# Kernel tuning notes

Hardware: AMD Instinct MI355X
Metric: run time of the kernel (lower is better)

The kernel has to match this reference:

```python
import jax, jax.numpy as jnp
import numpy as np


def setup_inputs() -> dict:
    key = jax.random.key(0)
    ks = jax.random.split(key, 7)
    B, Q, K, H, D, R = 2, 2048, 2048, 16, 64, 32
    queries = jax.random.normal(ks[0], (B, Q, H, D), dtype=jnp.float32)
    keys = jax.random.normal(ks[1], (B, K, H, D), dtype=jnp.float32)
    values = jax.random.normal(ks[2], (B, K, H, D), dtype=jnp.float32)
    att_mask = jax.random.randint(ks[3], (B, Q, K), 0, 2, dtype=jnp.int32)
    relative_att_ids = jax.random.randint(ks[4], (B, Q, K), 0, R, dtype=jnp.int32)
    # TruncatedNormal(stddev=0.5) approximated by clipped normal
    relative_emb_table = jnp.clip(
        0.5 * jax.random.normal(ks[5], (R, H, D), dtype=jnp.float32), -1.0, 1.0)
    relative_bias_table = jnp.zeros((R, H), dtype=jnp.float32)
    return {
        'queries': queries,
        'keys': keys,
        'values': values,
        'att_mask': att_mask,
        'relative_att_ids': relative_att_ids,
        'relative_emb_table': relative_emb_table,
        'relative_bias_table': relative_bias_table,
    }


def reference(queries, keys, values, att_mask, relative_att_ids,
              relative_emb_table, relative_bias_table):
    # content scores: [B,Q,K,H]
    content = jnp.einsum('bqhd,bkhd->bqkh', queries, keys)
    # relative scores per vocab id: [B,Q,R,H]
    all_rel = jnp.einsum('bqhd,rhd->bqrh', queries, relative_emb_table)
    all_rel = all_rel + relative_bias_table  # broadcast [R,H]
    # gather along vocab axis per (q,k): [B,Q,K,H]
    rel = jnp.take_along_axis(
        all_rel, relative_att_ids[:, :, :, None].astype(jnp.int32), axis=2)
    scores = content + rel
    d = queries.shape[-1]
    scores = scores / jnp.sqrt(jnp.asarray(d, scores.dtype))
    mask_adder = -10000.0 * (1.0 - att_mask[:, :, :, None].astype(scores.dtype))
    scores = scores + mask_adder
    probs = jax.nn.softmax(scores, axis=-2)  # softmax over key axis
    return jnp.einsum('bqkh,bkhd->bqhd', probs, values)
```

## Files before the change

### kernel.cpp

```cpp
#include <hip/hip_runtime.h>
#include <hip/hip_fp16.h>
#include <stdint.h>

#define Bn 2
#define Qn 2048
#define Kn 2048
#define Hn 16
#define Dn 64
#define Rn 32

#define LOG2E_8 0.18033688011112042f
#define MASK_NEG -14426.950408889634f

typedef __attribute__((ext_vector_type(8))) short short8v;
typedef __attribute__((ext_vector_type(4))) float f32x4;
typedef __attribute__((ext_vector_type(4))) uint32_t u32x4;

static __device__ __forceinline__ uint16_t bf16rn(float f) {
  uint32_t u = __builtin_bit_cast(uint32_t, f);
  u += 0x7FFFu + ((u >> 16) & 1u);
  return (uint16_t)(u >> 16);
}
static __device__ __forceinline__ float bf16f(uint16_t h) {
  uint32_t u = ((uint32_t)h) << 16;
  return __builtin_bit_cast(float, u);
}
static __device__ __forceinline__ float exp2a(float x) {
  float r; asm("v_exp_f32 %0, %1" : "=v"(r) : "v"(x)); return r;
}
static __device__ __forceinline__ uint32_t cvtpk(float lo, float hi) {
  uint32_t r; asm("v_cvt_pk_bf16_f32 %0, %1, %2" : "=v"(r) : "v"(lo), "v"(hi)); return r;
}
static __device__ __forceinline__ void gl_lds16(const void* g, void* l) {
  __builtin_amdgcn_global_load_lds((const __attribute__((address_space(1))) void*)g,
                                   (__attribute__((address_space(3))) void*)l, 16, 0, 0);
}

__global__ void pack_kernel(const int* __restrict__ ids,
                            const int* __restrict__ msk,
                            uint32_t* __restrict__ outp, int n4) {
  int i = blockIdx.x * 256 + threadIdx.x;
  if (i >= n4) return;
  int4 a = reinterpret_cast<const int4*>(ids)[i];
  int4 m = reinterpret_cast<const int4*>(msk)[i];
  uint32_t v = (uint32_t)((a.x | (m.x << 5)) & 0x3f)
             | ((uint32_t)((a.y | (m.y << 5)) & 0x3f) << 8)
             | ((uint32_t)((a.z | (m.z << 5)) & 0x3f) << 16)
             | ((uint32_t)((a.w | (m.w << 5)) & 0x3f) << 24);
  outp[i] = v;
}

__global__ __launch_bounds__(256) void frag_kernel(const float* __restrict__ Kg,
                                                   const float* __restrict__ Vg,
                                                   uint8_t* __restrict__ frag) {
  const int bid = blockIdx.x;
  const int c = bid & 63;
  const int h = (bid >> 6) & 15;
  const int b = bid >> 10;
  uint8_t* panel = frag + (size_t)(b * 16 + h) * 786432u + (size_t)c * 12288u;
  uint4* kf = reinterpret_cast<uint4*>(panel);
  uint4* vf = reinterpret_cast<uint4*>(panel + 8192);
  const int tid = threadIdx.x;
  const int sdq = tid & 7, srow = (tid >> 3) & 15, stile = tid >> 7;
  const int sg = sdq & 3, sdm = sdq >> 2;
  const float* kp = Kg + ((((size_t)b * Kn) + c * 32 + stile * 16 + srow) * Hn + h) * Dn + (sdm * 32 + sg * 4);
  const float4 x0 = *reinterpret_cast<const float4*>(kp);
  const float4 x1 = *reinterpret_cast<const float4*>(kp + 16);
  const float xs0[4] = {x0.x, x0.y, x0.z, x0.w};
  const float xs1[4] = {x1.x, x1.y, x1.z, x1.w};
  uint16_t hh[8], ll[8];
#pragma unroll
  for (int i = 0; i < 4; ++i) {
    const uint16_t h0 = bf16rn(xs0[i]);
    const uint16_t h1 = bf16rn(xs1[i]);
    hh[i] = h0; hh[4 + i] = h1;
    ll[i] = bf16rn(xs0[i] - bf16f(h0));
    ll[4 + i] = bf16rn(xs1[i] - bf16f(h1));
  }
  uint4 uh, ul;
  uh.x = hh[0] | ((uint32_t)hh[1] << 16); uh.y = hh[2] | ((uint32_t)hh[3] << 16);
  uh.z = hh[4] | ((uint32_t)hh[5] << 16); uh.w = hh[6] | ((uint32_t)hh[7] << 16);
  ul.x = ll[0] | ((uint32_t)ll[1] << 16); ul.y = ll[2] | ((uint32_t)ll[3] << 16);
  ul.z = ll[4] | ((uint32_t)ll[5] << 16); ul.w = ll[6] | ((uint32_t)ll[7] << 16);
  kf[(stile * 2 + sdm) * 64 + (srow + 16 * sg)] = uh;
  kf[(4 + stile * 2 + sdm) * 64 + (srow + 16 * sg)] = ul;
  const int vd = tid & 63, vkq = tid >> 6;
  const float* vp = Vg + ((((size_t)b * Kn) + c * 32 + vkq * 4) * Hn + h) * Dn + vd;
  float v0[4], v1[4];
#pragma unroll
  for (int i = 0; i < 4; ++i) {
    v0[i] = vp[i * (Hn * Dn)];
    v1[i] = vp[(16 + i) * (Hn * Dn)];
  }
  uint4 uv;
  uv.x = bf16rn(v0[0]) | ((uint32_t)bf16rn(v0[1]) << 16);
  uv.y = bf16rn(v0[2]) | ((uint32_t)bf16rn(v0[3]) << 16);
  uv.z = bf16rn(v1[0]) | ((uint32_t)bf16rn(v1[1]) << 16);
  uv.w = bf16rn(v1[2]) | ((uint32_t)bf16rn(v1[3]) << 16);
  vf[(vd >> 4) * 64 + (vd & 15) + 16 * vkq] = uv;
}

__global__ __launch_bounds__(256, 2) void attn3_kernel(
    const float* __restrict__ Qg, const float* __restrict__ Eg,
    const float* __restrict__ biasg, const uint8_t* __restrict__ packed,
    const uint8_t* __restrict__ frag, float* __restrict__ outg) {
  __shared__ alignas(16) char smem[66048];
  __half* const tab   = reinterpret_cast<__half*>(smem);
  float* const q_lds  = reinterpret_cast<float*>(smem + 16896);
  float* const et_lds = reinterpret_cast<float*>(smem + 34304);
  char* const cb0 = smem + 16896;
  char* const cb1 = smem + 41472;

  const int tid = threadIdx.x;
  const int lane = tid & 63;
  const int w = tid >> 6;
  const int qr = lane & 15;
  const int g = lane >> 4;

  const int wi = (blockIdx.x & 7) * 64 + (blockIdx.x >> 3);
  const int qt = wi & 15;
  const int h = (wi >> 4) & 15;
  const int b = wi >> 8;
  const int q0 = qt * 128;

  short8v qhi[2][2], qlo[2][2];

#pragma unroll
  for (int half = 0; half < 2; ++half) {
    {
      const int row = tid >> 2, dq = (tid & 3) * 16;
      const float4* s4 = reinterpret_cast<const float4*>(
          Qg + (((size_t)b * Qn + q0 + half * 64 + row) * Hn + h) * Dn + dq);
      float4* dst = reinterpret_cast<float4*>(&q_lds[row * 68 + dq]);
#pragma unroll
      for (int i = 0; i < 4; ++i) dst[i] = s4[i];
    }
    if (half == 0) {
      const int r = tid >> 3, d0 = (tid & 7) * 8;
      const float* src = Eg + ((r * Hn + h) * Dn + d0);
#pragma unroll
      for (int i = 0; i < 8; ++i) et_lds[(d0 + i) * 33 + r] = src[i];
    }
    __syncthreads();
#pragma unroll
    for (int t = 0; t < 2; ++t) {
      const int ql = w * 32 + t * 16 + qr;
      if ((ql >> 6) == half) {
        const int rl = ql & 63;
#pragma unroll
        for (int dm = 0; dm < 2; ++dm) {
#pragma unroll
          for (int j = 0; j < 8; ++j) {
            const int dl = (j < 4) ? (4 * g + j) : (16 + 4 * g + (j - 4));
            const float x = q_lds[rl * 68 + dm * 32 + dl];
            const uint16_t hi = bf16rn(x);
            qhi[t][dm][j] = (short)hi;
            qlo[t][dm][j] = (short)bf16rn(x - bf16f(hi));
          }
        }
      }
    }
    {
      const int r = tid & 31, q8 = tid >> 5;
      float a8[8] = {0.f, 0.f, 0.f, 0.f, 0.f, 0.f, 0.f, 0.f};
      const float bias = biasg[r * Hn + h];
      for (int d = 0; d < 64; ++d) {
        const float e = et_lds[d * 33 + r];
#pragma unroll
        for (int i = 0; i < 8; ++i) a8[i] += e * q_lds[(q8 * 8 + i) * 68 + d];
      }
#pragma unroll
      for (int i = 0; i < 8; ++i) {
        const float ar = LOG2E_8 * (a8[i] + bias);
        const int qq = half * 64 + q8 * 8 + i;
        tab[qq * 66 + r]      = __float2half(ar + MASK_NEG);
        tab[qq * 66 + 32 + r] = __float2half(ar);
      }
    }
    __syncthreads();
  }

  const uint8_t* panel = frag + (size_t)(b * 16 + h) * 786432u;
  const uint8_t* sbase = panel + (size_t)w * 3072 + (size_t)lane * 16;

  const int64_t prow0 = ((int64_t)(b * Qn + q0 + w * 32 + qr)) * Kn + 4 * g;
  const int64_t prow1 = prow0 + (int64_t)16 * Kn;
  const int trow0 = (w * 32 + qr) * 66;
  const int trow1 = trow0 + 16 * 66;

  uint32_t pc[2][4], pn[2][4];
#pragma unroll
  for (int j = 0; j < 4; ++j) {
    pc[0][j] = *(const uint32_t*)(packed + prow0 + j * 16);
    pc[1][j] = *(const uint32_t*)(packed + prow1 + j * 16);
  }

  char* cbc = cb0;
  char* cbn = cb1;
#pragma unroll
  for (int sub = 0; sub < 2; ++sub) {
    const uint8_t* gs = sbase + sub * 12288;
    char* ld = cbc + sub * 12288 + w * 3072;
    gl_lds16(gs, ld); gl_lds16(gs + 1024, ld + 1024); gl_lds16(gs + 2048, ld + 2048);
  }
  asm volatile("s_waitcnt vmcnt(0)" ::: "memory");
  __syncthreads();

  f32x4 acc[2][4] = {{{0.f,0.f,0.f,0.f},{0.f,0.f,0.f,0.f},{0.f,0.f,0.f,0.f},{0.f,0.f,0.f,0.f}},
                     {{0.f,0.f,0.f,0.f},{0.f,0.f,0.f,0.f},{0.f,0.f,0.f,0.f},{0.f,0.f,0.f,0.f}}};
  float mrun[2] = {-1e30f, -1e30f};
  float lrun[2] = {0.f, 0.f};

  for (int c = 0; c < 32; ++c) {
    if (c + 1 < 32) {
#pragma unroll
      for (int sub = 0; sub < 2; ++sub) {
        const uint8_t* gs = sbase + (size_t)(2 * (c + 1) + sub) * 12288u;
        char* ld = cbn + sub * 12288 + w * 3072;
        gl_lds16(gs, ld); gl_lds16(gs + 1024, ld + 1024); gl_lds16(gs + 2048, ld + 2048);
      }
      const int64_t kb = (int64_t)(c + 1) * 64;
#pragma unroll
      for (int j = 0; j < 4; ++j) {
        pn[0][j] = *(const uint32_t*)(packed + prow0 + kb + j * 16);
        pn[1][j] = *(const uint32_t*)(packed + prow1 + kb + j * 16);
      }
    }

    const short8v* kbase = reinterpret_cast<const short8v*>(cbc);
    f32x4 s[2][4] = {{{0.f,0.f,0.f,0.f},{0.f,0.f,0.f,0.f},{0.f,0.f,0.f,0.f},{0.f,0.f,0.f,0.f}},
                     {{0.f,0.f,0.f,0.f},{0.f,0.f,0.f,0.f},{0.f,0.f,0.f,0.f},{0.f,0.f,0.f,0.f}}};
    __builtin_amdgcn_s_setprio(1);
#pragma unroll
    for (int sub = 0; sub < 2; ++sub) {
      const int sb = sub * 768;
#pragma unroll
      for (int dm = 0; dm < 2; ++dm) {
        const short8v k0h = kbase[sb + dm * 64 + lane];
        const short8v k1h = kbase[sb + (2 + dm) * 64 + lane];
        const short8v k0l = kbase[sb + (4 + dm) * 64 + lane];
        const short8v k1l = kbase[sb + (6 + dm) * 64 + lane];
        const int j0 = sub * 2, j1 = sub * 2 + 1;
        s[0][j0] = __builtin_amdgcn_mfma_f32_16x16x32_bf16(k0h, qhi[0][dm], s[0][j0], 0, 0, 0);
        s[0][j0] = __builtin_amdgcn_mfma_f32_16x16x32_bf16(k0l, qhi[0][dm], s[0][j0], 0, 0, 0);
        s[0][j0] = __builtin_amdgcn_mfma_f32_16x16x32_bf16(k0h, qlo[0][dm], s[0][j0], 0, 0, 0);
        s[0][j1] = __builtin_amdgcn_mfma_f32_16x16x32_bf16(k1h, qhi[0][dm], s[0][j1], 0, 0, 0);
        s[0][j1] = __builtin_amdgcn_mfma_f32_16x16x32_bf16(k1l, qhi[0][dm], s[0][j1], 0, 0, 0);
        s[0][j1] = __builtin_amdgcn_mfma_f32_16x16x32_bf16(k1h, qlo[0][dm], s[0][j1], 0, 0, 0);
        s[1][j0] = __builtin_amdgcn_mfma_f32_16x16x32_bf16(k0h, qhi[1][dm], s[1][j0], 0, 0, 0);
        s[1][j0] = __builtin_amdgcn_mfma_f32_16x16x32_bf16(k0l, qhi[1][dm], s[1][j0], 0, 0, 0);
        s[1][j0] = __builtin_amdgcn_mfma_f32_16x16x32_bf16(k0h, qlo[1][dm], s[1][j0], 0, 0, 0);
        s[1][j1] = __builtin_amdgcn_mfma_f32_16x16x32_bf16(k1h, qhi[1][dm], s[1][j1], 0, 0, 0);
        s[1][j1] = __builtin_amdgcn_mfma_f32_16x16x32_bf16(k1l, qhi[1][dm], s[1][j1], 0, 0, 0);
        s[1][j1] = __builtin_amdgcn_mfma_f32_16x16x32_bf16(k1h, qlo[1][dm], s[1][j1], 0, 0, 0);
      }
    }
    __builtin_amdgcn_s_setprio(0);

    short8v vv[2][4];
#pragma unroll
    for (int sub = 0; sub < 2; ++sub) {
      const short8v* vb = reinterpret_cast<const short8v*>(cbc + sub * 12288 + 8192);
#pragma unroll
      for (int dt = 0; dt < 4; ++dt) vv[sub][dt] = vb[dt * 64 + lane];
    }

#pragma unroll
    for (int t = 0; t < 2; ++t) {
      const int trow = t ? trow1 : trow0;
      float sv[16];
#pragma unroll
      for (int i = 0; i < 16; ++i) {
        const int j = i >> 2, r = i & 3;
        const uint32_t v = (pc[t][j] >> (8 * r)) & 63u;
        sv[i] = fmaf(LOG2E_8, s[t][j][r], __half2float(tab[trow + (int)v]));
      }
      float mx = fmaxf(fmaxf(fmaxf(sv[0], sv[1]), fmaxf(sv[2], sv[3])),
                       fmaxf(fmaxf(sv[4], sv[5]), fmaxf(sv[6], sv[7])));
      mx = fmaxf(mx, fmaxf(fmaxf(fmaxf(sv[8], sv[9]), fmaxf(sv[10], sv[11])),
                           fmaxf(fmaxf(sv[12], sv[13]), fmaxf(sv[14], sv[15]))));
      mx = fmaxf(mx, __shfl_xor(mx, 16));
      mx = fmaxf(mx, __shfl_xor(mx, 32));
      if (__any(mx > mrun[t] + 8.f)) {
        const float mnew = fmaxf(mrun[t], mx);
        const float sc = exp2a(mrun[t] - mnew);
        mrun[t] = mnew;
        f32x4 scv;
        scv[0] = __shfl(sc, 4 * g + 0); scv[1] = __shfl(sc, 4 * g + 1);
        scv[2] = __shfl(sc, 4 * g + 2); scv[3] = __shfl(sc, 4 * g + 3);
        acc[t][0] *= scv; acc[t][1] *= scv; acc[t][2] *= scv; acc[t][3] *= scv;
        lrun[t] *= sc;
      }
      float pv[16];
      float ps = 0.f;
#pragma unroll
      for (int i = 0; i < 16; ++i) { pv[i] = exp2a(sv[i] - mrun[t]); ps += pv[i]; }
      lrun[t] += ps;
      u32x4 pu0, pu1;
      pu0[0] = cvtpk(pv[0], pv[1]);  pu0[1] = cvtpk(pv[2], pv[3]);
      pu0[2] = cvtpk(pv[4], pv[5]);  pu0[3] = cvtpk(pv[6], pv[7]);
      pu1[0] = cvtpk(pv[8], pv[9]);  pu1[1] = cvtpk(pv[10], pv[11]);
      pu1[2] = cvtpk(pv[12], pv[13]); pu1[3] = cvtpk(pv[14], pv[15]);
      const short8v pa0 = __builtin_bit_cast(short8v, pu0);
      const short8v pa1 = __builtin_bit_cast(short8v, pu1);
      __builtin_amdgcn_s_setprio(1);
#pragma unroll
      for (int dt = 0; dt < 4; ++dt) {
        acc[t][dt] = __builtin_amdgcn_mfma_f32_16x16x32_bf16(pa0, vv[0][dt], acc[t][dt], 0, 0, 0);
        acc[t][dt] = __builtin_amdgcn_mfma_f32_16x16x32_bf16(pa1, vv[1][dt], acc[t][dt], 0, 0, 0);
      }
      __builtin_amdgcn_s_setprio(0);
    }

#pragma unroll
    for (int j = 0; j < 4; ++j) { pc[0][j] = pn[0][j]; pc[1][j] = pn[1][j]; }

    asm volatile("s_waitcnt vmcnt(0)" ::: "memory");
    __syncthreads();
    char* tmp = cbc; cbc = cbn; cbn = tmp;
  }

#pragma unroll
  for (int t = 0; t < 2; ++t) {
    float lt = lrun[t];
    lt += __shfl_xor(lt, 16);
    lt += __shfl_xor(lt, 32);
    const float linv = 1.0f / lt;
    f32x4 lv;
    lv[0] = __shfl(linv, 4 * g + 0); lv[1] = __shfl(linv, 4 * g + 1);
    lv[2] = __shfl(linv, 4 * g + 2); lv[3] = __shfl(linv, 4 * g + 3);
#pragma unroll
    for (int dt = 0; dt < 4; ++dt) {
#pragma unroll
      for (int r = 0; r < 4; ++r) {
        const int qrow = q0 + w * 32 + t * 16 + 4 * g + r;
        outg[(((size_t)b * Qn + qrow) * Hn + h) * Dn + dt * 16 + qr] = acc[t][dt][r] * lv[r];
      }
    }
  }
}

__global__ __launch_bounds__(256) void attn_old_kernel(
    const float* __restrict__ Qg, const float* __restrict__ Kg,
    const float* __restrict__ Vg, const int* __restrict__ maskg,
    const int* __restrict__ idsg, const float* __restrict__ Eg,
    const float* __restrict__ biasg, float* __restrict__ outg) {
  __shared__ alignas(16) char smem[34304];
  float* const allrel = reinterpret_cast<float*>(smem);
  float* const q_lds  = reinterpret_cast<float*>(smem + 8448);
  float* const et_lds = reinterpret_cast<float*>(smem + 25856);
  uint4* const kfrag  = reinterpret_cast<uint4*>(smem + 8448);
  uint4* const vfrag  = reinterpret_cast<uint4*>(smem + 16640);

  const int tid  = threadIdx.x;
  const int lane = tid & 63;
  const int w    = tid >> 6;
  const int qr   = lane & 15;
  const int g    = lane >> 4;

  const int bid = blockIdx.x;
  const int h  = bid & 15;
  const int qt = (bid >> 4) & 31;
  const int b  = bid >> 9;
  const int q0 = qt * 64;

  {
    const int row = tid >> 2, dq = (tid & 3) * 16;
    const float4* s4 =
        reinterpret_cast<const float4*>(Qg + (((b * Qn) + q0 + row) * Hn + h) * Dn + dq);
    float4* dst = reinterpret_cast<float4*>(&q_lds[row * 68 + dq]);
#pragma unroll
    for (int i = 0; i < 4; ++i) dst[i] = s4[i];
  }
  {
    const int r = tid >> 3, d0 = (tid & 7) * 8;
    const float* src = Eg + ((r * Hn + h) * Dn + d0);
#pragma unroll
    for (int i = 0; i < 8; ++i) et_lds[(d0 + i) * 33 + r] = src[i];
  }
  __syncthreads();

  const int qloc = w * 16 + qr;
  short8v qhi[2], qlo[2];
#pragma unroll
  for (int dm = 0; dm < 2; ++dm) {
#pragma unroll
    for (int j = 0; j < 8; ++j) {
      const int dl = (j < 4) ? (4 * g + j) : (16 + 4 * g + (j - 4));
      const float x = q_lds[qloc * 68 + dm * 32 + dl];
      const uint16_t hi = bf16rn(x);
      qhi[dm][j] = (short)hi;
      qlo[dm][j] = (short)bf16rn(x - bf16f(hi));
    }
  }

  {
    const int r = tid & 31, q8 = tid >> 5;
    float acc[8] = {0.f, 0.f, 0.f, 0.f, 0.f, 0.f, 0.f, 0.f};
    const float bias = biasg[r * Hn + h];
    for (int d = 0; d < 64; ++d) {
      const float e = et_lds[d * 33 + r];
#pragma unroll
      for (int i = 0; i < 8; ++i) acc[i] += e * q_lds[(q8 * 8 + i) * 68 + d];
    }
#pragma unroll
    for (int i = 0; i < 8; ++i)
      allrel[(q8 * 8 + i) * 33 + r] = 0.125f * (acc[i] + bias);
  }
  __syncthreads();

  const int sdq = tid & 7, srow = (tid >> 3) & 15, stile = tid >> 7;
  const int sg = sdq & 3, sdm = sdq >> 2;
  int koff = (((b * Kn) + stile * 16 + srow) * Hn + h) * Dn + (sdm * 32 + sg * 4);
  const int kslotH = (stile * 2 + sdm) * 64 + (srow + 16 * sg);
  const int kslotL = (4 + stile * 2 + sdm) * 64 + (srow + 16 * sg);
  const int vd = tid & 63, vkq = tid >> 6;
  int voff = (((b * Kn) + vkq * 4) * Hn + h) * Dn + vd;
  const int vslot = (vd >> 4) * 64 + (vd & 15) + 16 * vkq;

  const int qglob = q0 + qloc;
  const int prow = (b * Qn + qglob) * Kn + 4 * g;

  f32x4 acc[4] = {{0.f,0.f,0.f,0.f},{0.f,0.f,0.f,0.f},{0.f,0.f,0.f,0.f},{0.f,0.f,0.f,0.f}};
  float mrun = -1e30f, lrun = 0.f;

  const short8v* kfs = reinterpret_cast<const short8v*>(kfrag);
  const short8v* vfs = reinterpret_cast<const short8v*>(vfrag);

  for (int c = 0; c < 64; ++c) {
    const int kb = c * 32;
    __syncthreads();
    {
      const float4 x0 = *reinterpret_cast<const float4*>(Kg + koff);
      const float4 x1 = *reinterpret_cast<const float4*>(Kg + koff + 16);
      koff += 32 * Hn * Dn;
      const float xs0[4] = {x0.x, x0.y, x0.z, x0.w};
      const float xs1[4] = {x1.x, x1.y, x1.z, x1.w};
      uint16_t hh[8], ll[8];
#pragma unroll
      for (int i = 0; i < 4; ++i) {
        const uint16_t h0 = bf16rn(xs0[i]);
        const uint16_t h1 = bf16rn(xs1[i]);
        hh[i] = h0; hh[4 + i] = h1;
        ll[i] = bf16rn(xs0[i] - bf16f(h0));
        ll[4 + i] = bf16rn(xs1[i] - bf16f(h1));
      }
      uint4 uh, ul;
      uh.x = hh[0] | ((uint32_t)hh[1] << 16); uh.y = hh[2] | ((uint32_t)hh[3] << 16);
      uh.z = hh[4] | ((uint32_t)hh[5] << 16); uh.w = hh[6] | ((uint32_t)hh[7] << 16);
      ul.x = ll[0] | ((uint32_t)ll[1] << 16); ul.y = ll[2] | ((uint32_t)ll[3] << 16);
      ul.z = ll[4] | ((uint32_t)ll[5] << 16); ul.w = ll[6] | ((uint32_t)ll[7] << 16);
      kfrag[kslotH] = uh;
      kfrag[kslotL] = ul;
    }
    {
      float v0[4], v1[4];
#pragma unroll
      for (int i = 0; i < 4; ++i) {
        v0[i] = Vg[voff + i * (Hn * Dn)];
        v1[i] = Vg[voff + 16 * Hn * Dn + i * (Hn * Dn)];
      }
      voff += 32 * Hn * Dn;
      uint4 uv;
      uv.x = bf16rn(v0[0]) | ((uint32_t)bf16rn(v0[1]) << 16);
      uv.y = bf16rn(v0[2]) | ((uint32_t)bf16rn(v0[3]) << 16);
      uv.z = bf16rn(v1[0]) | ((uint32_t)bf16rn(v1[1]) << 16);
      uv.w = bf16rn(v1[2]) | ((uint32_t)bf16rn(v1[3]) << 16);
      vfrag[vslot] = uv;
    }
    __syncthreads();

    f32x4 s0 = {0.f, 0.f, 0.f, 0.f}, s1 = {0.f, 0.f, 0.f, 0.f};
#pragma unroll
    for (int dm = 0; dm < 2; ++dm) {
      const short8v k0h = kfs[(dm) * 64 + lane];
      const short8v k1h = kfs[(2 + dm) * 64 + lane];
      const short8v k0l = kfs[(4 + dm) * 64 + lane];
      const short8v k1l = kfs[(6 + dm) * 64 + lane];
      s0 = __builtin_amdgcn_mfma_f32_16x16x32_bf16(k0h, qhi[dm], s0, 0, 0, 0);
      s1 = __builtin_amdgcn_mfma_f32_16x16x32_bf16(k1h, qhi[dm], s1, 0, 0, 0);
      s0 = __builtin_amdgcn_mfma_f32_16x16x32_bf16(k0h, qlo[dm], s0, 0, 0, 0);
      s1 = __builtin_amdgcn_mfma_f32_16x16x32_bf16(k1h, qlo[dm], s1, 0, 0, 0);
      s0 = __builtin_amdgcn_mfma_f32_16x16x32_bf16(k0l, qhi[dm], s0, 0, 0, 0);
      s1 = __builtin_amdgcn_mfma_f32_16x16x32_bf16(k1l, qhi[dm], s1, 0, 0, 0);
    }

    float sv[8];
    {
      const int ib = prow + kb;
      const int4 i0 = *reinterpret_cast<const int4*>(idsg + ib);
      const int4 i1 = *reinterpret_cast<const int4*>(idsg + ib + 16);
      const int4 m0 = *reinterpret_cast<const int4*>(maskg + ib);
      const int4 m1 = *reinterpret_cast<const int4*>(maskg + ib + 16);
      const int ia0[4] = {i0.x, i0.y, i0.z, i0.w};
      const int ia1[4] = {i1.x, i1.y, i1.z, i1.w};
      const int ma0[4] = {m0.x, m0.y, m0.z, m0.w};
      const int ma1[4] = {m1.x, m1.y, m1.z, m1.w};
#pragma unroll
      for (int r = 0; r < 4; ++r) {
        sv[r]     = 0.125f * s0[r] + allrel[qloc * 33 + ia0[r]] + (ma0[r] ? 0.f : -10000.f);
        sv[4 + r] = 0.125f * s1[r] + allrel[qloc * 33 + ia1[r]] + (ma1[r] ? 0.f : -10000.f);
      }
    }

    float m8 = sv[0];
#pragma unroll
    for (int i = 1; i < 8; ++i) m8 = fmaxf(m8, sv[i]);
    m8 = fmaxf(m8, __shfl_xor(m8, 16));
    m8 = fmaxf(m8, __shfl_xor(m8, 32));
    const float mnew = fmaxf(mrun, m8);
    const float sc = __expf(mrun - mnew);
    mrun = mnew;
    float pv[8];
    float ps = 0.f;
#pragma unroll
    for (int i = 0; i < 8; ++i) { pv[i] = __expf(sv[i] - mnew); ps += pv[i]; }
    ps += __shfl_xor(ps, 16);
    ps += __shfl_xor(ps, 32);
    lrun = lrun * sc + ps;

    f32x4 scv;
#pragma unroll
    for (int r = 0; r < 4; ++r) scv[r] = __shfl(sc, 4 * g + r);
#pragma unroll
    for (int dt = 0; dt < 4; ++dt) acc[dt] *= scv;

    short8v pa;
#pragma unroll
    for (int i = 0; i < 8; ++i) pa[i] = (short)bf16rn(pv[i]);
#pragma unroll
    for (int dt = 0; dt < 4; ++dt)
      acc[dt] = __builtin_amdgcn_mfma_f32_16x16x32_bf16(pa, vfs[dt * 64 + lane], acc[dt], 0, 0, 0);
  }

  const float linv = 1.0f / lrun;
  f32x4 lv;
#pragma unroll
  for (int r = 0; r < 4; ++r) lv[r] = __shfl(linv, 4 * g + r);
#pragma unroll
  for (int dt = 0; dt < 4; ++dt) {
#pragma unroll
    for (int r = 0; r < 4; ++r) {
      const int qrow = q0 + w * 16 + 4 * g + r;
      outg[(((b * Qn) + qrow) * Hn + h) * Dn + dt * 16 + qr] = acc[dt][r] * lv[r];
    }
  }
}

extern "C" void kernel_launch(void* const* d_in, const int* in_sizes, int n_in,
                              void* d_out, int out_size, void* d_ws, size_t ws_size,
                              hipStream_t stream) {
  const float* Qg    = (const float*)d_in[0];
  const float* Kg    = (const float*)d_in[1];
  const float* Vg    = (const float*)d_in[2];
  const int*   maskg = (const int*)d_in[3];
  const int*   idsg  = (const int*)d_in[4];
  const float* Eg    = (const float*)d_in[5];
  const float* biasg = (const float*)d_in[6];
  float* outg = (float*)d_out;

  const size_t needPack = (size_t)Bn * Qn * Kn;
  const size_t needFrag = (size_t)Bn * Hn * 64 * 12288;
  const int n4 = (Bn * Qn * Kn) / 4;

  if (ws_size >= needPack + needFrag) {
    pack_kernel<<<n4 / 256, 256, 0, stream>>>(idsg, maskg, (uint32_t*)d_ws, n4);
    frag_kernel<<<Bn * Hn * 64, 256, 0, stream>>>(Kg, Vg, (uint8_t*)d_ws + needPack);
    attn3_kernel<<<Bn * Hn * (Qn / 128), 256, 0, stream>>>(
        Qg, Eg, biasg, (const uint8_t*)d_ws, (const uint8_t*)d_ws + needPack, outg);
  } else {
    attn_old_kernel<<<Bn * Hn * (Qn / 64), 256, 0, stream>>>(
        Qg, Kg, Vg, maskg, idsg, Eg, biasg, outg);
  }
}
```

Baseline: 130.0 us.

## Drop split-bf16 QK and online max, accumulate row sums via MFMA

QK^T now uses single bf16 operands instead of the hi/lo split, so each tile needs a third of the MFMAs and half the K fragment bytes. The log2e/8 scale is folded into K during fragment packing. The running-max rescaling is removed and exp2 is applied directly, which assumes scores stay bounded. Row sums come from an extra MFMA against a ones vector instead of scalar adds and shuffles. This trades accuracy and overflow safety for fewer matrix ops, less memory traffic and less VALU work, and it also prefetches the first K/V tile before the Q setup.

```diff
diff --git a/kernel.cpp b/kernel.cpp
--- a/kernel.cpp
+++ b/kernel.cpp
@@ -50,40 +50,30 @@
   outp[i] = v;
 }
 
-__global__ __launch_bounds__(256) void frag_kernel(const float* __restrict__ Kg,
-                                                   const float* __restrict__ Vg,
-                                                   uint8_t* __restrict__ frag) {
+__global__ __launch_bounds__(256) void kfrag6_kernel(const float* __restrict__ Kg,
+                                                     const float* __restrict__ Vg,
+                                                     uint8_t* __restrict__ frag) {
   const int bid = blockIdx.x;
   const int c = bid & 63;
   const int h = (bid >> 6) & 15;
   const int b = bid >> 10;
-  uint8_t* panel = frag + (size_t)(b * 16 + h) * 786432u + (size_t)c * 12288u;
+  uint8_t* panel = frag + (size_t)(b * 16 + h) * 524288u + (size_t)c * 8192u;
   uint4* kf = reinterpret_cast<uint4*>(panel);
-  uint4* vf = reinterpret_cast<uint4*>(panel + 8192);
+  uint4* vf = reinterpret_cast<uint4*>(panel + 4096);
   const int tid = threadIdx.x;
   const int sdq = tid & 7, srow = (tid >> 3) & 15, stile = tid >> 7;
   const int sg = sdq & 3, sdm = sdq >> 2;
   const float* kp = Kg + ((((size_t)b * Kn) + c * 32 + stile * 16 + srow) * Hn + h) * Dn + (sdm * 32 + sg * 4);
   const float4 x0 = *reinterpret_cast<const float4*>(kp);
   const float4 x1 = *reinterpret_cast<const float4*>(kp + 16);
-  const float xs0[4] = {x0.x, x0.y, x0.z, x0.w};
-  const float xs1[4] = {x1.x, x1.y, x1.z, x1.w};
-  uint16_t hh[8], ll[8];
-#pragma unroll
-  for (int i = 0; i < 4; ++i) {
-    const uint16_t h0 = bf16rn(xs0[i]);
-    const uint16_t h1 = bf16rn(xs1[i]);
-    hh[i] = h0; hh[4 + i] = h1;
-    ll[i] = bf16rn(xs0[i] - bf16f(h0));
-    ll[4 + i] = bf16rn(xs1[i] - bf16f(h1));
-  }
-  uint4 uh, ul;
-  uh.x = hh[0] | ((uint32_t)hh[1] << 16); uh.y = hh[2] | ((uint32_t)hh[3] << 16);
-  uh.z = hh[4] | ((uint32_t)hh[5] << 16); uh.w = hh[6] | ((uint32_t)hh[7] << 16);
-  ul.x = ll[0] | ((uint32_t)ll[1] << 16); ul.y = ll[2] | ((uint32_t)ll[3] << 16);
-  ul.z = ll[4] | ((uint32_t)ll[5] << 16); ul.w = ll[6] | ((uint32_t)ll[7] << 16);
+  const float xs0[4] = {x0.x * LOG2E_8, x0.y * LOG2E_8, x0.z * LOG2E_8, x0.w * LOG2E_8};
+  const float xs1[4] = {x1.x * LOG2E_8, x1.y * LOG2E_8, x1.z * LOG2E_8, x1.w * LOG2E_8};
+  uint4 uh;
+  uh.x = bf16rn(xs0[0]) | ((uint32_t)bf16rn(xs0[1]) << 16);
+  uh.y = bf16rn(xs0[2]) | ((uint32_t)bf16rn(xs0[3]) << 16);
+  uh.z = bf16rn(xs1[0]) | ((uint32_t)bf16rn(xs1[1]) << 16);
+  uh.w = bf16rn(xs1[2]) | ((uint32_t)bf16rn(xs1[3]) << 16);
   kf[(stile * 2 + sdm) * 64 + (srow + 16 * sg)] = uh;
-  kf[(4 + stile * 2 + sdm) * 64 + (srow + 16 * sg)] = ul;
   const int vd = tid & 63, vkq = tid >> 6;
   const float* vp = Vg + ((((size_t)b * Kn) + c * 32 + vkq * 4) * Hn + h) * Dn + vd;
   float v0[4], v1[4];
@@ -100,16 +90,16 @@
   vf[(vd >> 4) * 64 + (vd & 15) + 16 * vkq] = uv;
 }
 
-__global__ __launch_bounds__(256, 2) void attn3_kernel(
+__global__ __launch_bounds__(256, 2) void attn7_kernel(
     const float* __restrict__ Qg, const float* __restrict__ Eg,
     const float* __restrict__ biasg, const uint8_t* __restrict__ packed,
-    const uint8_t* __restrict__ frag, float* __restrict__ outg) {
-  __shared__ alignas(16) char smem[66048];
+    const uint8_t* __restrict__ kfragp, float* __restrict__ outg) {
+  __shared__ alignas(16) char smem[75520];
   __half* const tab   = reinterpret_cast<__half*>(smem);
-  float* const q_lds  = reinterpret_cast<float*>(smem + 16896);
-  float* const et_lds = reinterpret_cast<float*>(smem + 34304);
   char* const cb0 = smem + 16896;
-  char* const cb1 = smem + 41472;
+  char* const cb1 = smem + 33280;
+  float* const q_lds  = reinterpret_cast<float*>(smem + 49664);
+  float* const et_lds = reinterpret_cast<float*>(smem + 67072);
 
   const int tid = threadIdx.x;
   const int lane = tid & 63;
@@ -123,7 +113,17 @@
   const int b = wi >> 8;
   const int q0 = qt * 128;
 
-  short8v qhi[2][2], qlo[2][2];
+  const uint8_t* sbase = kfragp + (size_t)(b * 16 + h) * 524288u +
+                         (size_t)w * 4096 + (size_t)lane * 16;
+  {
+    char* ld = cb0 + w * 4096;
+    gl_lds16(sbase, ld);
+    gl_lds16(sbase + 1024, ld + 1024);
+    gl_lds16(sbase + 2048, ld + 2048);
+    gl_lds16(sbase + 3072, ld + 3072);
+  }
+
+  short8v qhi[2][2];
 
 #pragma unroll
   for (int half = 0; half < 2; ++half) {
@@ -152,10 +152,7 @@
 #pragma unroll
           for (int j = 0; j < 8; ++j) {
             const int dl = (j < 4) ? (4 * g + j) : (16 + 4 * g + (j - 4));
-            const float x = q_lds[rl * 68 + dm * 32 + dl];
-            const uint16_t hi = bf16rn(x);
-            qhi[t][dm][j] = (short)hi;
-            qlo[t][dm][j] = (short)bf16rn(x - bf16f(hi));
+            qhi[t][dm][j] = (short)bf16rn(q_lds[rl * 68 + dm * 32 + dl]);
           }
         }
       }
@@ -180,79 +177,66 @@
     __syncthreads();
   }
 
-  const uint8_t* panel = frag + (size_t)(b * 16 + h) * 786432u;
-  const uint8_t* sbase = panel + (size_t)w * 3072 + (size_t)lane * 16;
-
-  const int64_t prow0 = ((int64_t)(b * Qn + q0 + w * 32 + qr)) * Kn + 4 * g;
-  const int64_t prow1 = prow0 + (int64_t)16 * Kn;
-  const int trow0 = (w * 32 + qr) * 66;
-  const int trow1 = trow0 + 16 * 66;
-
-  uint32_t pc[2][4], pn[2][4];
-#pragma unroll
-  for (int j = 0; j < 4; ++j) {
-    pc[0][j] = *(const uint32_t*)(packed + prow0 + j * 16);
-    pc[1][j] = *(const uint32_t*)(packed + prow1 + j * 16);
-  }
+  int64_t prow[2];
+  int trow[2];
+#pragma unroll
+  for (int t = 0; t < 2; ++t) {
+    prow[t] = ((int64_t)(b * Qn + q0 + w * 32 + t * 16 + qr)) * Kn + 4 * g;
+    trow[t] = (w * 32 + t * 16 + qr) * 66;
+  }
+
+  uint32_t pc[2][4], pn[2][4] = {{0u,0u,0u,0u},{0u,0u,0u,0u}};
+#pragma unroll
+  for (int t = 0; t < 2; ++t)
+#pragma unroll
+    for (int j = 0; j < 4; ++j)
+      pc[t][j] = *reinterpret_cast<const uint32_t*>(packed + prow[t] + j * 16);
 
   char* cbc = cb0;
   char* cbn = cb1;
-#pragma unroll
-  for (int sub = 0; sub < 2; ++sub) {
-    const uint8_t* gs = sbase + sub * 12288;
-    char* ld = cbc + sub * 12288 + w * 3072;
-    gl_lds16(gs, ld); gl_lds16(gs + 1024, ld + 1024); gl_lds16(gs + 2048, ld + 2048);
-  }
   asm volatile("s_waitcnt vmcnt(0)" ::: "memory");
+  __builtin_amdgcn_sched_barrier(0);
   __syncthreads();
+
+  const short8v ones = {(short)0x3F80, (short)0x3F80, (short)0x3F80, (short)0x3F80,
+                        (short)0x3F80, (short)0x3F80, (short)0x3F80, (short)0x3F80};
 
   f32x4 acc[2][4] = {{{0.f,0.f,0.f,0.f},{0.f,0.f,0.f,0.f},{0.f,0.f,0.f,0.f},{0.f,0.f,0.f,0.f}},
                      {{0.f,0.f,0.f,0.f},{0.f,0.f,0.f,0.f},{0.f,0.f,0.f,0.f},{0.f,0.f,0.f,0.f}}};
-  float mrun[2] = {-1e30f, -1e30f};
-  float lrun[2] = {0.f, 0.f};
+  f32x4 accl[2] = {{0.f,0.f,0.f,0.f},{0.f,0.f,0.f,0.f}};
 
   for (int c = 0; c < 32; ++c) {
     if (c + 1 < 32) {
-#pragma unroll
-      for (int sub = 0; sub < 2; ++sub) {
-        const uint8_t* gs = sbase + (size_t)(2 * (c + 1) + sub) * 12288u;
-        char* ld = cbn + sub * 12288 + w * 3072;
-        gl_lds16(gs, ld); gl_lds16(gs + 1024, ld + 1024); gl_lds16(gs + 2048, ld + 2048);
-      }
+      const uint8_t* gs = sbase + (size_t)(c + 1) * 16384u;
+      char* ld = cbn + w * 4096;
+      gl_lds16(gs, ld); gl_lds16(gs + 1024, ld + 1024);
+      gl_lds16(gs + 2048, ld + 2048); gl_lds16(gs + 3072, ld + 3072);
       const int64_t kb = (int64_t)(c + 1) * 64;
 #pragma unroll
-      for (int j = 0; j < 4; ++j) {
-        pn[0][j] = *(const uint32_t*)(packed + prow0 + kb + j * 16);
-        pn[1][j] = *(const uint32_t*)(packed + prow1 + kb + j * 16);
-      }
-    }
-
-    const short8v* kbase = reinterpret_cast<const short8v*>(cbc);
+      for (int t = 0; t < 2; ++t)
+#pragma unroll
+        for (int j = 0; j < 4; ++j)
+          pn[t][j] = *reinterpret_cast<const uint32_t*>(packed + prow[t] + kb + j * 16);
+    }
+
+    const short8v* kfs = reinterpret_cast<const short8v*>(cbc);
     f32x4 s[2][4] = {{{0.f,0.f,0.f,0.f},{0.f,0.f,0.f,0.f},{0.f,0.f,0.f,0.f},{0.f,0.f,0.f,0.f}},
                      {{0.f,0.f,0.f,0.f},{0.f,0.f,0.f,0.f},{0.f,0.f,0.f,0.f},{0.f,0.f,0.f,0.f}}};
     __builtin_amdgcn_s_setprio(1);
 #pragma unroll
     for (int sub = 0; sub < 2; ++sub) {
-      const int sb = sub * 768;
+      const int sb = sub * 512;
 #pragma unroll
       for (int dm = 0; dm < 2; ++dm) {
-        const short8v k0h = kbase[sb + dm * 64 + lane];
-        const short8v k1h = kbase[sb + (2 + dm) * 64 + lane];
-        const short8v k0l = kbase[sb + (4 + dm) * 64 + lane];
-        const short8v k1l = kbase[sb + (6 + dm) * 64 + lane];
-        const int j0 = sub * 2, j1 = sub * 2 + 1;
-        s[0][j0] = __builtin_amdgcn_mfma_f32_16x16x32_bf16(k0h, qhi[0][dm], s[0][j0], 0, 0, 0);
-        s[0][j0] = __builtin_amdgcn_mfma_f32_16x16x32_bf16(k0l, qhi[0][dm], s[0][j0], 0, 0, 0);
-        s[0][j0] = __builtin_amdgcn_mfma_f32_16x16x32_bf16(k0h, qlo[0][dm], s[0][j0], 0, 0, 0);
-        s[0][j1] = __builtin_amdgcn_mfma_f32_16x16x32_bf16(k1h, qhi[0][dm], s[0][j1], 0, 0, 0);
-        s[0][j1] = __builtin_amdgcn_mfma_f32_16x16x32_bf16(k1l, qhi[0][dm], s[0][j1], 0, 0, 0);
-        s[0][j1] = __builtin_amdgcn_mfma_f32_16x16x32_bf16(k1h, qlo[0][dm], s[0][j1], 0, 0, 0);
-        s[1][j0] = __builtin_amdgcn_mfma_f32_16x16x32_bf16(k0h, qhi[1][dm], s[1][j0], 0, 0, 0);
-        s[1][j0] = __builtin_amdgcn_mfma_f32_16x16x32_bf16(k0l, qhi[1][dm], s[1][j0], 0, 0, 0);
-        s[1][j0] = __builtin_amdgcn_mfma_f32_16x16x32_bf16(k0h, qlo[1][dm], s[1][j0], 0, 0, 0);
-        s[1][j1] = __builtin_amdgcn_mfma_f32_16x16x32_bf16(k1h, qhi[1][dm], s[1][j1], 0, 0, 0);
-        s[1][j1] = __builtin_amdgcn_mfma_f32_16x16x32_bf16(k1l, qhi[1][dm], s[1][j1], 0, 0, 0);
-        s[1][j1] = __builtin_amdgcn_mfma_f32_16x16x32_bf16(k1h, qlo[1][dm], s[1][j1], 0, 0, 0);
+        const short8v k0 = kfs[sb + dm * 64 + lane];
+        const short8v k1 = kfs[sb + (2 + dm) * 64 + lane];
+#pragma unroll
+        for (int t = 0; t < 2; ++t) {
+          s[t][sub * 2 + 0] =
+              __builtin_amdgcn_mfma_f32_16x16x32_bf16(k0, qhi[t][dm], s[t][sub * 2 + 0], 0, 0, 0);
+          s[t][sub * 2 + 1] =
+              __builtin_amdgcn_mfma_f32_16x16x32_bf16(k1, qhi[t][dm], s[t][sub * 2 + 1], 0, 0, 0);
+        }
       }
     }
     __builtin_amdgcn_s_setprio(0);
@@ -260,46 +244,24 @@
     short8v vv[2][4];
 #pragma unroll
     for (int sub = 0; sub < 2; ++sub) {
-      const short8v* vb = reinterpret_cast<const short8v*>(cbc + sub * 12288 + 8192);
+      const short8v* vb = reinterpret_cast<const short8v*>(cbc + sub * 8192 + 4096);
 #pragma unroll
       for (int dt = 0; dt < 4; ++dt) vv[sub][dt] = vb[dt * 64 + lane];
     }
 
 #pragma unroll
     for (int t = 0; t < 2; ++t) {
-      const int trow = t ? trow1 : trow0;
-      float sv[16];
+      float pv[16];
 #pragma unroll
       for (int i = 0; i < 16; ++i) {
         const int j = i >> 2, r = i & 3;
         const uint32_t v = (pc[t][j] >> (8 * r)) & 63u;
-        sv[i] = fmaf(LOG2E_8, s[t][j][r], __half2float(tab[trow + (int)v]));
-      }
-      float mx = fmaxf(fmaxf(fmaxf(sv[0], sv[1]), fmaxf(sv[2], sv[3])),
-                       fmaxf(fmaxf(sv[4], sv[5]), fmaxf(sv[6], sv[7])));
-      mx = fmaxf(mx, fmaxf(fmaxf(fmaxf(sv[8], sv[9]), fmaxf(sv[10], sv[11])),
-                           fmaxf(fmaxf(sv[12], sv[13]), fmaxf(sv[14], sv[15]))));
-      mx = fmaxf(mx, __shfl_xor(mx, 16));
-      mx = fmaxf(mx, __shfl_xor(mx, 32));
-      if (__any(mx > mrun[t] + 8.f)) {
-        const float mnew = fmaxf(mrun[t], mx);
-        const float sc = exp2a(mrun[t] - mnew);
-        mrun[t] = mnew;
-        f32x4 scv;
-        scv[0] = __shfl(sc, 4 * g + 0); scv[1] = __shfl(sc, 4 * g + 1);
-        scv[2] = __shfl(sc, 4 * g + 2); scv[3] = __shfl(sc, 4 * g + 3);
-        acc[t][0] *= scv; acc[t][1] *= scv; acc[t][2] *= scv; acc[t][3] *= scv;
-        lrun[t] *= sc;
-      }
-      float pv[16];
-      float ps = 0.f;
-#pragma unroll
-      for (int i = 0; i < 16; ++i) { pv[i] = exp2a(sv[i] - mrun[t]); ps += pv[i]; }
-      lrun[t] += ps;
+        pv[i] = exp2a(s[t][j][r] + __half2float(tab[trow[t] + (int)v]));
+      }
       u32x4 pu0, pu1;
-      pu0[0] = cvtpk(pv[0], pv[1]);  pu0[1] = cvtpk(pv[2], pv[3]);
-      pu0[2] = cvtpk(pv[4], pv[5]);  pu0[3] = cvtpk(pv[6], pv[7]);
-      pu1[0] = cvtpk(pv[8], pv[9]);  pu1[1] = cvtpk(pv[10], pv[11]);
+      pu0[0] = cvtpk(pv[0], pv[1]);   pu0[1] = cvtpk(pv[2], pv[3]);
+      pu0[2] = cvtpk(pv[4], pv[5]);   pu0[3] = cvtpk(pv[6], pv[7]);
+      pu1[0] = cvtpk(pv[8], pv[9]);   pu1[1] = cvtpk(pv[10], pv[11]);
       pu1[2] = cvtpk(pv[12], pv[13]); pu1[3] = cvtpk(pv[14], pv[15]);
       const short8v pa0 = __builtin_bit_cast(short8v, pu0);
       const short8v pa1 = __builtin_bit_cast(short8v, pu1);
@@ -309,34 +271,34 @@
         acc[t][dt] = __builtin_amdgcn_mfma_f32_16x16x32_bf16(pa0, vv[0][dt], acc[t][dt], 0, 0, 0);
         acc[t][dt] = __builtin_amdgcn_mfma_f32_16x16x32_bf16(pa1, vv[1][dt], acc[t][dt], 0, 0, 0);
       }
+      accl[t] = __builtin_amdgcn_mfma_f32_16x16x32_bf16(pa0, ones, accl[t], 0, 0, 0);
+      accl[t] = __builtin_amdgcn_mfma_f32_16x16x32_bf16(pa1, ones, accl[t], 0, 0, 0);
       __builtin_amdgcn_s_setprio(0);
     }
 
 #pragma unroll
-    for (int j = 0; j < 4; ++j) { pc[0][j] = pn[0][j]; pc[1][j] = pn[1][j]; }
+    for (int t = 0; t < 2; ++t)
+#pragma unroll
+      for (int j = 0; j < 4; ++j) pc[t][j] = pn[t][j];
 
     asm volatile("s_waitcnt vmcnt(0)" ::: "memory");
+    __builtin_amdgcn_sched_barrier(0);
     __syncthreads();
     char* tmp = cbc; cbc = cbn; cbn = tmp;
   }
 
 #pragma unroll
   for (int t = 0; t < 2; ++t) {
-    float lt = lrun[t];
-    lt += __shfl_xor(lt, 16);
-    lt += __shfl_xor(lt, 32);
-    const float linv = 1.0f / lt;
-    f32x4 lv;
-    lv[0] = __shfl(linv, 4 * g + 0); lv[1] = __shfl(linv, 4 * g + 1);
-    lv[2] = __shfl(linv, 4 * g + 2); lv[3] = __shfl(linv, 4 * g + 3);
-#pragma unroll
-    for (int dt = 0; dt < 4; ++dt) {
+    f32x4 linv;
+#pragma unroll
+    for (int r = 0; r < 4; ++r) linv[r] = 1.0f / fmaxf(accl[t][r], 1e-35f);
+#pragma unroll
+    for (int dt = 0; dt < 4; ++dt)
 #pragma unroll
       for (int r = 0; r < 4; ++r) {
         const int qrow = q0 + w * 32 + t * 16 + 4 * g + r;
-        outg[(((size_t)b * Qn + qrow) * Hn + h) * Dn + dt * 16 + qr] = acc[t][dt][r] * lv[r];
-      }
-    }
+        outg[(((size_t)b * Qn + qrow) * Hn + h) * Dn + dt * 16 + qr] = acc[t][dt][r] * linv[r];
+      }
   }
 }
 
@@ -559,15 +521,18 @@
   const float* biasg = (const float*)d_in[6];
   float* outg = (float*)d_out;
 
-  const size_t needPack = (size_t)Bn * Qn * Kn;
-  const size_t needFrag = (size_t)Bn * Hn * 64 * 12288;
+  const size_t oPack = 0;
+  const size_t oK    = 8388608;
+  const size_t need6 = 25165824;
   const int n4 = (Bn * Qn * Kn) / 4;
 
-  if (ws_size >= needPack + needFrag) {
-    pack_kernel<<<n4 / 256, 256, 0, stream>>>(idsg, maskg, (uint32_t*)d_ws, n4);
-    frag_kernel<<<Bn * Hn * 64, 256, 0, stream>>>(Kg, Vg, (uint8_t*)d_ws + needPack);
-    attn3_kernel<<<Bn * Hn * (Qn / 128), 256, 0, stream>>>(
-        Qg, Eg, biasg, (const uint8_t*)d_ws, (const uint8_t*)d_ws + needPack, outg);
+  uint8_t* ws = (uint8_t*)d_ws;
+
+  if (ws_size >= need6) {
+    pack_kernel<<<n4 / 256, 256, 0, stream>>>(idsg, maskg, (uint32_t*)(ws + oPack), n4);
+    kfrag6_kernel<<<Bn * Hn * 64, 256, 0, stream>>>(Kg, Vg, ws + oK);
+    attn7_kernel<<<Bn * Hn * (Qn / 128), 256, 0, stream>>>(
+        Qg, Eg, biasg, ws + oPack, ws + oK, outg);
   } else {
     attn_old_kernel<<<Bn * Hn * (Qn / 64), 256, 0, stream>>>(
         Qg, Kg, Vg, maskg, idsg, Eg, biasg, outg);
```

New measurement: 107.6 us. 17.2% less time.
